# Kernel tuning notes

Hardware: AMD Instinct MI355X
Metric: run time of the kernel (lower is better)

## Reference

```python
import jax, jax.numpy as jnp
import numpy as np

BETA = 0.95
THR = 1.0
SLOPE = 25.0


@jax.custom_vjp
def spike(x):
    # Heaviside spike with fast-sigmoid surrogate gradient (snntorch fast_sigmoid, slope=25)
    return (x > 0).astype(x.dtype)

def _spike_fwd(x):
    return spike(x), x

def _spike_bwd(x, g):
    sg = 1.0 / (SLOPE * jnp.abs(x) + 1.0) ** 2
    return (g * sg,)

spike.defvjp(_spike_fwd, _spike_bwd)


def setup_inputs() -> dict:
    key = jax.random.key(0)
    k_x, k_w1, k_b1, k_w2, k_b2 = jax.random.split(key, 5)
    T, B, D_IN, H, OUT = 30, 4096, 784, 128, 10
    x = jax.random.uniform(k_x, (T, B, D_IN), dtype=jnp.float32)
    # PyTorch nn.Linear default init: U(-1/sqrt(fan_in), 1/sqrt(fan_in))
    lim1 = 1.0 / np.sqrt(D_IN)
    lim2 = 1.0 / np.sqrt(H)
    W1 = jax.random.uniform(k_w1, (H, D_IN), jnp.float32, -lim1, lim1)
    b1 = jax.random.uniform(k_b1, (H,), jnp.float32, -lim1, lim1)
    W2 = jax.random.uniform(k_w2, (OUT, H), jnp.float32, -lim2, lim2)
    b2 = jax.random.uniform(k_b2, (OUT,), jnp.float32, -lim2, lim2)
    return {"x": x, "W1": W1, "b1": b1, "W2": W2, "b2": b2}


def reference(x, W1, b1, W2, b2):
    T, B, _ = x.shape
    H, OUT = W1.shape[0], W2.shape[0]

    def step(carry, xt):
        mem1, mem2 = carry
        # layer 1: linear + leaky integrate-and-fire (reset by subtraction)
        cur1 = xt @ W1.T + b1  # [B, H]
        reset1 = jax.lax.stop_gradient((mem1 - THR > 0).astype(xt.dtype))
        mem1 = BETA * mem1 + cur1 - reset1 * THR
        spk1 = spike(mem1 - THR)
        # layer 2
        cur2 = spk1 @ W2.T + b2  # [B, OUT]
        reset2 = jax.lax.stop_gradient((mem2 - THR > 0).astype(xt.dtype))
        mem2 = BETA * mem2 + cur2 - reset2 * THR
        spk2 = spike(mem2 - THR)
        return (mem1, mem2), (spk2, mem2)

    init = (jnp.zeros((B, H), x.dtype), jnp.zeros((B, OUT), x.dtype))
    _, (spk2_rec, mem2_rec) = jax.lax.scan(step, init, x)
    return spk2_rec, mem2_rec  # each [T, B, OUT]
```

## Files before the change

kernel.cpp:

```cpp
#include <hip/hip_runtime.h>
#include <stdint.h>

#define THR  1.0f
#define BETA 0.95f
#define SX   4096.0f
#define SW   512.0f
#define SINV (1.0f / (4096.0f * 512.0f))
#define W1N  (128 * 784)

typedef __attribute__((ext_vector_type(8)))  _Float16 f16x8;
typedef __attribute__((ext_vector_type(16))) float    f32x16;
typedef __attribute__((ext_vector_type(4)))  float    fvec4;

__device__ __forceinline__ void gll16(const float* g, float* l){
  __builtin_amdgcn_global_load_lds((const __attribute__((address_space(1))) void*)g,
                                   (__attribute__((address_space(3))) void*)l, 16, 0, 0);
}

__global__ void split_w1(const float* __restrict__ W1, _Float16* __restrict__ wB){
  int i = blockIdx.x * 256 + threadIdx.x;
  if (i < W1N) {
    int h = i / 784, k = i % 784;
    float v = W1[i] * SW;
    _Float16 hi = (_Float16)v;
    _Float16 lo = (_Float16)(v - (float)hi);
    int ks = k >> 4, kg = (k >> 3) & 1, j = k & 7, nf = h >> 5, r = h & 31;
    int base = ((ks * 4 + nf) * 2) * 512 + (kg * 32 + r) * 8 + j;
    wB[base]       = hi;
    wB[base + 512] = lo;
  }
}

__launch_bounds__(256, 2)
__global__ void gemm1(const float* __restrict__ x,
                      const float* __restrict__ wBf,
                      const float* __restrict__ b1,
                      float* __restrict__ cur1,
                      long row0){
  __shared__ float lds[20480];
  const int lane = threadIdx.x & 63;
  const int w    = threadIdx.x >> 6;
  const long blk_row0 = row0 + (long)blockIdx.x * 128;
  const int r  = lane & 31;
  const int kg = lane >> 5;
  const int row_a = w * 32 + r;
  const int xr  = (row_a & 7) << 4;
  const int xr3 = (row_a & 3) << 4;

  #define STAGE_A(bb, s) {                                                   \
    _Pragma("unroll") for (int i = 0; i < 4; ++i) {                          \
      int j = w * 4 + i;                                                     \
      int jj = j * 64 + lane;                                   \
      int rw = jj >> 3, q = (jj & 7) << 4;                                   \
      int kb = q ^ ((rw & 7) << 4);                                          \
      gll16(x + (blk_row0 + rw) * 784 + (s) * 32 + (kb >> 2),                \
            &lds[(bb) * 4096 + j * 256]); } }

  #define STAGE_B(bb, p) {                                                   \
    _Pragma("unroll") for (int i = 0; i < 4; ++i) {                          \
      int j = w * 4 + i;                                                     \
      gll16(wBf + (p) * 4096 + j * 256 + lane * 4,                           \
            &lds[8192 + (bb) * 4096 + j * 256]); } }

  #define COMPUTE(bb) {                                                      \
    _Pragma("unroll") for (int ksl = 0; ksl < 2; ++ksl) {                    \
      f16x8 b[8];                                                            \
      _Pragma("unroll") for (int f = 0; f < 8; ++f)                          \
        b[f] = *(const f16x8*)&lds[8192 + (bb) * 4096 + (ksl * 8 + f) * 256 + lane * 4]; \
      int kb0 = ksl * 64 + kg * 32;                                          \
      fvec4 a0 = *(const fvec4*)&lds[(bb) * 4096 + row_a * 32 + (((kb0)      ^ xr) >> 2)]; \
      fvec4 a1 = *(const fvec4*)&lds[(bb) * 4096 + row_a * 32 + (((kb0 + 16) ^ xr) >> 2)]; \
      f16x8 ah, al;                                                          \
      _Pragma("unroll") for (int j = 0; j < 8; ++j) {                        \
        float v = ((j < 4) ? a0[j] : a1[j - 4]) * SX;                        \
        _Float16 hh = (_Float16)v;                                           \
        ah[j] = hh; al[j] = (_Float16)(v - (float)hh);                       \
      }                                                                      \
      _Pragma("unroll") for (int nf = 0; nf < 4; ++nf) {                     \
        acc[nf] = __builtin_amdgcn_mfma_f32_32x32x16_f16(ah, b[nf * 2],     acc[nf], 0, 0, 0); \
        acc[nf] = __builtin_amdgcn_mfma_f32_32x32x16_f16(ah, b[nf * 2 + 1], acc[nf], 0, 0, 0); \
        acc[nf] = __builtin_amdgcn_mfma_f32_32x32x16_f16(al, b[nf * 2],     acc[nf], 0, 0, 0); \
      } } }

  #define FENCE_A() { __builtin_amdgcn_sched_barrier(0);                     \
    asm volatile("s_waitcnt lgkmcnt(0)" ::: "memory");                       \
    __builtin_amdgcn_s_barrier();                                            \
    asm volatile("" ::: "memory"); }
  #define FENCE_B(vm) {                                                      \
    asm volatile("s_waitcnt vmcnt(" #vm ")" ::: "memory");                   \
    __builtin_amdgcn_s_barrier();                                            \
    asm volatile("" ::: "memory");                                           \
    __builtin_amdgcn_sched_barrier(0); }

  f32x16 acc[4] = {};

  #pragma unroll
  for (int i = 0; i < 2; ++i) {
    int j = w * 2 + i;
    int jj = j * 64 + lane;
    int rw = jj >> 2, q = (jj & 3) << 4;
    int kb = q ^ ((rw & 3) << 4);
    gll16(x + (blk_row0 + rw) * 784 + 768 + (kb >> 2), &lds[16384 + j * 256]);
    gll16(wBf + 98304 + j * 256 + lane * 4,            &lds[18432 + j * 256]);
  }
  STAGE_A(0, 0); STAGE_B(0, 0);
  STAGE_A(1, 1); STAGE_B(1, 1);
  FENCE_B(8);
  COMPUTE(0);

  for (int q = 0; q < 11; ++q) {
    const int p1 = 2 * q + 1;
    FENCE_A();
    STAGE_A(0, p1 + 1); STAGE_B(0, p1 + 1);
    FENCE_B(8);
    COMPUTE(1);
    const int p2 = 2 * q + 2;
    FENCE_A();
    STAGE_A(1, p2 + 1); STAGE_B(1, p2 + 1);
    FENCE_B(8);
    COMPUTE(0);
  }

  FENCE_A();
  FENCE_B(0);
  COMPUTE(1);

  {
    f16x8 b[8];
    #pragma unroll
    for (int f = 0; f < 8; ++f)
      b[f] = *(const f16x8*)&lds[18432 + f * 256 + lane * 4];
    int kb0 = kg * 32;
    fvec4 a0 = *(const fvec4*)&lds[16384 + row_a * 16 + (((kb0)      ^ xr3) >> 2)];
    fvec4 a1 = *(const fvec4*)&lds[16384 + row_a * 16 + (((kb0 + 16) ^ xr3) >> 2)];
    f16x8 ah, al;
    #pragma unroll
    for (int j = 0; j < 8; ++j) {
      float v = ((j < 4) ? a0[j] : a1[j - 4]) * SX;
      _Float16 hh = (_Float16)v;
      ah[j] = hh; al[j] = (_Float16)(v - (float)hh);
    }
    #pragma unroll
    for (int nf = 0; nf < 4; ++nf) {
      acc[nf] = __builtin_amdgcn_mfma_f32_32x32x16_f16(ah, b[nf * 2],     acc[nf], 0, 0, 0);
      acc[nf] = __builtin_amdgcn_mfma_f32_32x32x16_f16(ah, b[nf * 2 + 1], acc[nf], 0, 0, 0);
      acc[nf] = __builtin_amdgcn_mfma_f32_32x32x16_f16(al, b[nf * 2],     acc[nf], 0, 0, 0);
    }
  }

  float b1v[4];
  #pragma unroll
  for (int nf = 0; nf < 4; ++nf) b1v[nf] = b1[nf * 32 + r];
  long m0 = (long)blockIdx.x * 128 + w * 32;
  #pragma unroll
  for (int nf = 0; nf < 4; ++nf)
    #pragma unroll
    for (int reg = 0; reg < 16; ++reg) {
      int rr = (reg & 3) + 8 * (reg >> 2) + 4 * kg;
      cur1[(m0 + rr) * 128 + nf * 32 + r] = acc[nf][reg] * SINV + b1v[nf];
    }
  #undef STAGE_A
  #undef STAGE_B
  #undef COMPUTE
  #undef FENCE_A
  #undef FENCE_B
}

__launch_bounds__(256)
__global__ void lif(const float* __restrict__ cur1,
                    const float* __restrict__ W2,
                    const float* __restrict__ b2,
                    float* __restrict__ out,
                    float* __restrict__ state1,
                    float* __restrict__ state2,
                    int t0, int tn){
  const int lane = threadIdx.x & 63;
  const int b = blockIdx.x * 4 + (threadIdx.x >> 6);
  const int o = lane & 15;
  const int c = lane >> 4;

  float wv[32];
  #pragma unroll
  for (int j = 0; j < 32; ++j) wv[j] = 0.f;
  if (o < 10) {
    #pragma unroll
    for (int j = 0; j < 32; ++j) wv[j] = W2[o * 128 + c * 32 + j];
  }
  float b2v = (lane < 10) ? b2[lane] : 0.f;

  float mem1a, mem1b, mem2;
  if (t0 == 0) { mem1a = 0.f; mem1b = 0.f; mem2 = 0.f; }
  else {
    mem1a = state1[b * 128 + lane];
    mem1b = state1[b * 128 + 64 + lane];
    mem2  = (lane < 10) ? state2[b * 10 + lane] : 0.f;
  }

  for (int t = t0; t < tn; ++t) {
    long base = ((long)(t - t0) * 4096 + b) * 128;
    float c1a = cur1[base + lane];
    float c1b = cur1[base + 64 + lane];
    float r1a = (mem1a > THR) ? THR : 0.f;
    float r1b = (mem1b > THR) ? THR : 0.f;
    mem1a = BETA * mem1a + c1a - r1a;
    mem1b = BETA * mem1b + c1b - r1b;

    uint64_t mA = __ballot(mem1a > THR);
    uint64_t mB = __ballot(mem1b > THR);
    uint64_t m64 = (c & 2) ? mB : mA;
    uint32_t bits = (uint32_t)(m64 >> ((c & 1) << 5));

    float s = 0.f;
    #pragma unroll
    for (int j = 0; j < 32; ++j)
      s = fmaf((float)((bits >> j) & 1u), wv[j], s);
    s += __shfl_xor(s, 16);
    s += __shfl_xor(s, 32);

    if (lane < 10) {
      float cur2 = s + b2v;
      float r2 = (mem2 > THR) ? THR : 0.f;
      mem2 = BETA * mem2 + cur2 - r2;
      float s2 = (mem2 > THR) ? 1.f : 0.f;
      long ob = (long)t * 40960 + (long)b * 10 + lane;
      out[ob] = s2;
      out[1228800 + ob] = mem2;
    }
  }

  if (tn < 30) {
    state1[b * 128 + lane] = mem1a;
    state1[b * 128 + 64 + lane] = mem1b;
    if (lane < 10) state2[b * 10 + lane] = mem2;
  }
}

extern "C" void kernel_launch(void* const* d_in, const int* in_sizes, int n_in,
                              void* d_out, int out_size, void* d_ws, size_t ws_size,
                              hipStream_t stream) {
  const float* x  = (const float*)d_in[0];
  const float* W1 = (const float*)d_in[1];
  const float* b1 = (const float*)d_in[2];
  const float* W2 = (const float*)d_in[3];
  const float* b2 = (const float*)d_in[4];
  float* out = (float*)d_out;

  const int T = 30, B = 4096;

  char* ws = (char*)d_ws;
  _Float16* wB = (_Float16*)ws;
  size_t off = (size_t)49 * 8 * 512 * sizeof(_Float16);
  off = (off + 255) & ~(size_t)255;
  float* state1 = (float*)(ws + off); off += (size_t)B * 128 * 4;
  float* state2 = (float*)(ws + off); off += (size_t)B * 10 * 4;
  off = (off + 255) & ~(size_t)255;
  float* cur1 = (float*)(ws + off);

  size_t per_t = (size_t)B * 128 * 4;
  size_t avail = (ws_size > off) ? (ws_size - off) : 0;
  int CH = (int)(avail / per_t);
  if (CH > T) CH = T;
  if (CH < 1) CH = 1;

  split_w1<<<(W1N + 255) / 256, 256, 0, stream>>>(W1, wB);

  for (int t0 = 0; t0 < T; t0 += CH) {
    int tn = (t0 + CH < T) ? (t0 + CH) : T;
    int mrows = (tn - t0) * B;
    gemm1<<<mrows / 128, 256, 0, stream>>>(x, (const float*)wB, b1, cur1, (long)t0 * B);
    lif<<<B / 4, 256, 0, stream>>>(cur1, W2, b2, out, state1, state2, t0, tn);
  }
}
```

Measured before the change: 144.7 us.

## Use four-stage K16 pipeline with direct per-lane A loads in gemm1

Replaces the double-buffered K=32 staging (swizzled A tiles plus a separate tail chunk) with a 4-deep ring of K=16 stages, where each lane loads its own A row fragment straight into LDS in MFMA-ready order. This removes the XOR-swizzle address math and the special K-tail path, and keeps more loads in flight to hide global latency. In exchange there are twice as many barrier rounds per K, smaller 16-byte strided row loads from x, and a lower LDS footprint.

```diff
diff --git a/kernel.cpp b/kernel.cpp
--- a/kernel.cpp
+++ b/kernel.cpp
@@ -37,50 +37,39 @@
                       const float* __restrict__ b1,
                       float* __restrict__ cur1,
                       long row0){
-  __shared__ float lds[20480];
+  __shared__ float lds[16384];
   const int lane = threadIdx.x & 63;
   const int w    = threadIdx.x >> 6;
   const long blk_row0 = row0 + (long)blockIdx.x * 128;
   const int r  = lane & 31;
   const int kg = lane >> 5;
-  const int row_a = w * 32 + r;
-  const int xr  = (row_a & 7) << 4;
-  const int xr3 = (row_a & 3) << 4;
-
-  #define STAGE_A(bb, s) {                                                   \
-    _Pragma("unroll") for (int i = 0; i < 4; ++i) {                          \
-      int j = w * 4 + i;                                                     \
-      int jj = j * 64 + lane;                                   \
-      int rw = jj >> 3, q = (jj & 7) << 4;                                   \
-      int kb = q ^ ((rw & 7) << 4);                                          \
-      gll16(x + (blk_row0 + rw) * 784 + (s) * 32 + (kb >> 2),                \
-            &lds[(bb) * 4096 + j * 256]); } }
-
-  #define STAGE_B(bb, p) {                                                   \
-    _Pragma("unroll") for (int i = 0; i < 4; ++i) {                          \
-      int j = w * 4 + i;                                                     \
-      gll16(wBf + (p) * 4096 + j * 256 + lane * 4,                           \
-            &lds[8192 + (bb) * 4096 + j * 256]); } }
+
+  const float* xA  = x + (blk_row0 + w * 32 + r) * 784 + kg * 8;
+  const float* wBs = wBf + w * 512 + lane * 4;
+
+  #define STAGE(bb, s) {                                                     \
+    gll16(xA  + (s) * 16,       &lds[(bb) * 4096 + (w * 2 + 0) * 256]);      \
+    gll16(xA  + (s) * 16 + 4,   &lds[(bb) * 4096 + (w * 2 + 1) * 256]);      \
+    gll16(wBs + (s) * 2048,     &lds[(bb) * 4096 + 2048 + (w * 2 + 0) * 256]); \
+    gll16(wBs + (s) * 2048 + 256, &lds[(bb) * 4096 + 2048 + (w * 2 + 1) * 256]); }
 
   #define COMPUTE(bb) {                                                      \
-    _Pragma("unroll") for (int ksl = 0; ksl < 2; ++ksl) {                    \
-      f16x8 b[8];                                                            \
-      _Pragma("unroll") for (int f = 0; f < 8; ++f)                          \
-        b[f] = *(const f16x8*)&lds[8192 + (bb) * 4096 + (ksl * 8 + f) * 256 + lane * 4]; \
-      int kb0 = ksl * 64 + kg * 32;                                          \
-      fvec4 a0 = *(const fvec4*)&lds[(bb) * 4096 + row_a * 32 + (((kb0)      ^ xr) >> 2)]; \
-      fvec4 a1 = *(const fvec4*)&lds[(bb) * 4096 + row_a * 32 + (((kb0 + 16) ^ xr) >> 2)]; \
-      f16x8 ah, al;                                                          \
-      _Pragma("unroll") for (int j = 0; j < 8; ++j) {                        \
-        float v = ((j < 4) ? a0[j] : a1[j - 4]) * SX;                        \
-        _Float16 hh = (_Float16)v;                                           \
-        ah[j] = hh; al[j] = (_Float16)(v - (float)hh);                       \
-      }                                                                      \
-      _Pragma("unroll") for (int nf = 0; nf < 4; ++nf) {                     \
-        acc[nf] = __builtin_amdgcn_mfma_f32_32x32x16_f16(ah, b[nf * 2],     acc[nf], 0, 0, 0); \
-        acc[nf] = __builtin_amdgcn_mfma_f32_32x32x16_f16(ah, b[nf * 2 + 1], acc[nf], 0, 0, 0); \
-        acc[nf] = __builtin_amdgcn_mfma_f32_32x32x16_f16(al, b[nf * 2],     acc[nf], 0, 0, 0); \
-      } } }
+    f16x8 b[8];                                                              \
+    _Pragma("unroll") for (int f = 0; f < 8; ++f)                            \
+      b[f] = *(const f16x8*)&lds[(bb) * 4096 + 2048 + f * 256 + lane * 4];   \
+    fvec4 a0 = *(const fvec4*)&lds[(bb) * 4096 + (w * 2 + 0) * 256 + lane * 4]; \
+    fvec4 a1 = *(const fvec4*)&lds[(bb) * 4096 + (w * 2 + 1) * 256 + lane * 4]; \
+    f16x8 ah, al;                                                            \
+    _Pragma("unroll") for (int j = 0; j < 8; ++j) {                          \
+      float v = ((j < 4) ? a0[j] : a1[j - 4]) * SX;                          \
+      _Float16 hh = (_Float16)v;                                             \
+      ah[j] = hh; al[j] = (_Float16)(v - (float)hh);                         \
+    }                                                                        \
+    _Pragma("unroll") for (int nf = 0; nf < 4; ++nf) {                       \
+      acc[nf] = __builtin_amdgcn_mfma_f32_32x32x16_f16(ah, b[nf * 2],     acc[nf], 0, 0, 0); \
+      acc[nf] = __builtin_amdgcn_mfma_f32_32x32x16_f16(ah, b[nf * 2 + 1], acc[nf], 0, 0, 0); \
+      acc[nf] = __builtin_amdgcn_mfma_f32_32x32x16_f16(al, b[nf * 2],     acc[nf], 0, 0, 0); \
+    } }
 
   #define FENCE_A() { __builtin_amdgcn_sched_barrier(0);                     \
     asm volatile("s_waitcnt lgkmcnt(0)" ::: "memory");                       \
@@ -94,59 +83,22 @@
 
   f32x16 acc[4] = {};
 
-  #pragma unroll
-  for (int i = 0; i < 2; ++i) {
-    int j = w * 2 + i;
-    int jj = j * 64 + lane;
-    int rw = jj >> 2, q = (jj & 3) << 4;
-    int kb = q ^ ((rw & 3) << 4);
-    gll16(x + (blk_row0 + rw) * 784 + 768 + (kb >> 2), &lds[16384 + j * 256]);
-    gll16(wBf + 98304 + j * 256 + lane * 4,            &lds[18432 + j * 256]);
-  }
-  STAGE_A(0, 0); STAGE_B(0, 0);
-  STAGE_A(1, 1); STAGE_B(1, 1);
-  FENCE_B(8);
+  STAGE(0, 0); STAGE(1, 1); STAGE(2, 2); STAGE(3, 3);
+  FENCE_B(12);
   COMPUTE(0);
 
   for (int q = 0; q < 11; ++q) {
-    const int p1 = 2 * q + 1;
-    FENCE_A();
-    STAGE_A(0, p1 + 1); STAGE_B(0, p1 + 1);
-    FENCE_B(8);
-    COMPUTE(1);
-    const int p2 = 2 * q + 2;
-    FENCE_A();
-    STAGE_A(1, p2 + 1); STAGE_B(1, p2 + 1);
-    FENCE_B(8);
-    COMPUTE(0);
-  }
-
-  FENCE_A();
-  FENCE_B(0);
-  COMPUTE(1);
-
-  {
-    f16x8 b[8];
-    #pragma unroll
-    for (int f = 0; f < 8; ++f)
-      b[f] = *(const f16x8*)&lds[18432 + f * 256 + lane * 4];
-    int kb0 = kg * 32;
-    fvec4 a0 = *(const fvec4*)&lds[16384 + row_a * 16 + (((kb0)      ^ xr3) >> 2)];
-    fvec4 a1 = *(const fvec4*)&lds[16384 + row_a * 16 + (((kb0 + 16) ^ xr3) >> 2)];
-    f16x8 ah, al;
-    #pragma unroll
-    for (int j = 0; j < 8; ++j) {
-      float v = ((j < 4) ? a0[j] : a1[j - 4]) * SX;
-      _Float16 hh = (_Float16)v;
-      ah[j] = hh; al[j] = (_Float16)(v - (float)hh);
-    }
-    #pragma unroll
-    for (int nf = 0; nf < 4; ++nf) {
-      acc[nf] = __builtin_amdgcn_mfma_f32_32x32x16_f16(ah, b[nf * 2],     acc[nf], 0, 0, 0);
-      acc[nf] = __builtin_amdgcn_mfma_f32_32x32x16_f16(ah, b[nf * 2 + 1], acc[nf], 0, 0, 0);
-      acc[nf] = __builtin_amdgcn_mfma_f32_32x32x16_f16(al, b[nf * 2],     acc[nf], 0, 0, 0);
-    }
-  }
+    const int s = 4 * q + 1;
+    FENCE_A(); STAGE(0, s + 3); FENCE_B(12); COMPUTE(1);
+    FENCE_A(); STAGE(1, s + 4); FENCE_B(12); COMPUTE(2);
+    FENCE_A(); STAGE(2, s + 5); FENCE_B(12); COMPUTE(3);
+    FENCE_A(); STAGE(3, s + 6); FENCE_B(12); COMPUTE(0);
+  }
+
+  FENCE_A(); STAGE(0, 48); FENCE_B(12); COMPUTE(1);
+  FENCE_A();               FENCE_B(8);  COMPUTE(2);
+  FENCE_A();               FENCE_B(4);  COMPUTE(3);
+  FENCE_A();               FENCE_B(0);  COMPUTE(0);
 
   float b1v[4];
   #pragma unroll
@@ -159,8 +111,7 @@
       int rr = (reg & 3) + 8 * (reg >> 2) + 4 * kg;
       cur1[(m0 + rr) * 128 + nf * 32 + r] = acc[nf][reg] * SINV + b1v[nf];
     }
-  #undef STAGE_A
-  #undef STAGE_B
+  #undef STAGE
   #undef COMPUTE
   #undef FENCE_A
   #undef FENCE_B
```

Measured after the change: 172.4 us. 1.19x slower.

## Enlarge gemm1 tile to 256 rows with 8 waves in a 4x2 warp grid

Applied to the files above, without the earlier changes.

The layer-1 GEMM block grows from 128 to 256 rows and from 4 to 8 waves. The waves form a 4x2 grid where each wave computes a 64x64 sub-tile, so every staged W1 tile in LDS is shared by twice as many rows of x. This cuts W1 staging traffic and LDS B-fragment reads per output. In exchange it uses more LDS per block, halves the number of blocks, and changes per-wave register pressure, which may reduce occupancy or latency hiding.

```diff
diff --git a/kernel.cpp b/kernel.cpp
--- a/kernel.cpp
+++ b/kernel.cpp
@@ -31,56 +31,62 @@
   }
 }
 
-__launch_bounds__(256, 2)
+__launch_bounds__(512, 2)
 __global__ void gemm1(const float* __restrict__ x,
                       const float* __restrict__ wBf,
                       const float* __restrict__ b1,
                       float* __restrict__ cur1,
                       long row0){
-  __shared__ float lds[20480];
+  __shared__ float lds[30720];
   const int lane = threadIdx.x & 63;
   const int w    = threadIdx.x >> 6;
-  const long blk_row0 = row0 + (long)blockIdx.x * 128;
+  const int wm   = w >> 1;
+  const int wn   = w & 1;
+  const long blk_row0 = row0 + (long)blockIdx.x * 256;
   const int r  = lane & 31;
   const int kg = lane >> 5;
-  const int row_a = w * 32 + r;
-  const int xr  = (row_a & 7) << 4;
-  const int xr3 = (row_a & 3) << 4;
-
-  #define STAGE_A(bb, s) {                                                   \
-    _Pragma("unroll") for (int i = 0; i < 4; ++i) {                          \
-      int j = w * 4 + i;                                                     \
+  const int row_a = wm * 64;
+
+  #define STAGE_A(p, s) { _Pragma("unroll") for (int i = 0; i < 4; ++i) {    \
+      int j = w * 4 + i;                                          \
       int jj = j * 64 + lane;                                   \
       int rw = jj >> 3, q = (jj & 7) << 4;                                   \
       int kb = q ^ ((rw & 7) << 4);                                          \
       gll16(x + (blk_row0 + rw) * 784 + (s) * 32 + (kb >> 2),                \
-            &lds[(bb) * 4096 + j * 256]); } }
-
-  #define STAGE_B(bb, p) {                                                   \
-    _Pragma("unroll") for (int i = 0; i < 4; ++i) {                          \
-      int j = w * 4 + i;                                                     \
-      gll16(wBf + (p) * 4096 + j * 256 + lane * 4,                           \
-            &lds[8192 + (bb) * 4096 + j * 256]); } }
-
-  #define COMPUTE(bb) {                                                      \
-    _Pragma("unroll") for (int ksl = 0; ksl < 2; ++ksl) {                    \
-      f16x8 b[8];                                                            \
-      _Pragma("unroll") for (int f = 0; f < 8; ++f)                          \
-        b[f] = *(const f16x8*)&lds[8192 + (bb) * 4096 + (ksl * 8 + f) * 256 + lane * 4]; \
-      int kb0 = ksl * 64 + kg * 32;                                          \
-      fvec4 a0 = *(const fvec4*)&lds[(bb) * 4096 + row_a * 32 + (((kb0)      ^ xr) >> 2)]; \
-      fvec4 a1 = *(const fvec4*)&lds[(bb) * 4096 + row_a * 32 + (((kb0 + 16) ^ xr) >> 2)]; \
+            &lds[(p) * 8192 + j * 256]); } }
+
+  #define STAGE_B(p, s) { _Pragma("unroll") for (int i = 0; i < 2; ++i) {    \
+      int j = w * 2 + i;                                          \
+      gll16(wBf + (s) * 4096 + j * 256 + lane * 4,                           \
+            &lds[16384 + (p) * 4096 + j * 256]); } }
+
+  #define STAGE(p, s) { STAGE_A(p, s); STAGE_B(p, s); }
+
+  #define KSTEP(p, ksl) {                                                    \
+    f16x8 b[4];                                                              \
+    _Pragma("unroll") for (int nfl = 0; nfl < 2; ++nfl)                      \
+      _Pragma("unroll") for (int t = 0; t < 2; ++t)                          \
+        b[nfl * 2 + t] = *(const f16x8*)&lds[16384 + (p) * 4096 +            \
+            ((ksl) * 8 + (wn * 2 + nfl) * 2 + t) * 256 + lane * 4];          \
+    _Pragma("unroll") for (int mf = 0; mf < 2; ++mf) {                       \
+      int ra = row_a + mf * 32 + r;                                          \
+      int xr = (ra & 7) << 4;                                                \
+      int kb0 = (ksl) * 64 + kg * 32;                                        \
+      fvec4 a0 = *(const fvec4*)&lds[(p) * 8192 + ra * 32 + (((kb0)      ^ xr) >> 2)]; \
+      fvec4 a1 = *(const fvec4*)&lds[(p) * 8192 + ra * 32 + (((kb0 + 16) ^ xr) >> 2)]; \
       f16x8 ah, al;                                                          \
       _Pragma("unroll") for (int j = 0; j < 8; ++j) {                        \
         float v = ((j < 4) ? a0[j] : a1[j - 4]) * SX;                        \
         _Float16 hh = (_Float16)v;                                           \
         ah[j] = hh; al[j] = (_Float16)(v - (float)hh);                       \
       }                                                                      \
-      _Pragma("unroll") for (int nf = 0; nf < 4; ++nf) {                     \
-        acc[nf] = __builtin_amdgcn_mfma_f32_32x32x16_f16(ah, b[nf * 2],     acc[nf], 0, 0, 0); \
-        acc[nf] = __builtin_amdgcn_mfma_f32_32x32x16_f16(ah, b[nf * 2 + 1], acc[nf], 0, 0, 0); \
-        acc[nf] = __builtin_amdgcn_mfma_f32_32x32x16_f16(al, b[nf * 2],     acc[nf], 0, 0, 0); \
+      _Pragma("unroll") for (int nfl = 0; nfl < 2; ++nfl) {                  \
+        acc[mf * 2 + nfl] = __builtin_amdgcn_mfma_f32_32x32x16_f16(ah, b[nfl * 2],     acc[mf * 2 + nfl], 0, 0, 0); \
+        acc[mf * 2 + nfl] = __builtin_amdgcn_mfma_f32_32x32x16_f16(ah, b[nfl * 2 + 1], acc[mf * 2 + nfl], 0, 0, 0); \
+        acc[mf * 2 + nfl] = __builtin_amdgcn_mfma_f32_32x32x16_f16(al, b[nfl * 2],     acc[mf * 2 + nfl], 0, 0, 0); \
       } } }
+
+  #define CPH(p) { KSTEP(p, 0); KSTEP(p, 1); }
 
   #define FENCE_A() { __builtin_amdgcn_sched_barrier(0);                     \
     asm volatile("s_waitcnt lgkmcnt(0)" ::: "memory");                       \
@@ -100,68 +106,71 @@
     int jj = j * 64 + lane;
     int rw = jj >> 2, q = (jj & 3) << 4;
     int kb = q ^ ((rw & 3) << 4);
-    gll16(x + (blk_row0 + rw) * 784 + 768 + (kb >> 2), &lds[16384 + j * 256]);
-    gll16(wBf + 98304 + j * 256 + lane * 4,            &lds[18432 + j * 256]);
-  }
-  STAGE_A(0, 0); STAGE_B(0, 0);
-  STAGE_A(1, 1); STAGE_B(1, 1);
-  FENCE_B(8);
-  COMPUTE(0);
+    gll16(x + (blk_row0 + rw) * 784 + 768 + (kb >> 2), &lds[24576 + j * 256]);
+  }
+  gll16(wBf + 24 * 4096 + w * 256 + lane * 4, &lds[28672 + w * 256]);
+  STAGE(0, 0);
+  STAGE(1, 1);
+  FENCE_B(6);
+  CPH(0);
 
   for (int q = 0; q < 11; ++q) {
-    const int p1 = 2 * q + 1;
-    FENCE_A();
-    STAGE_A(0, p1 + 1); STAGE_B(0, p1 + 1);
-    FENCE_B(8);
-    COMPUTE(1);
-    const int p2 = 2 * q + 2;
-    FENCE_A();
-    STAGE_A(1, p2 + 1); STAGE_B(1, p2 + 1);
-    FENCE_B(8);
-    COMPUTE(0);
-  }
-
+    const int s = 2 * q + 1;
+    FENCE_A(); STAGE(0, s + 1); FENCE_B(6); CPH(1);
+    FENCE_A(); STAGE(1, s + 2); FENCE_B(6); CPH(0);
+  }
   FENCE_A();
   FENCE_B(0);
-  COMPUTE(1);
-
+  CPH(1);
   {
-    f16x8 b[8];
-    #pragma unroll
-    for (int f = 0; f < 8; ++f)
-      b[f] = *(const f16x8*)&lds[18432 + f * 256 + lane * 4];
-    int kb0 = kg * 32;
-    fvec4 a0 = *(const fvec4*)&lds[16384 + row_a * 16 + (((kb0)      ^ xr3) >> 2)];
-    fvec4 a1 = *(const fvec4*)&lds[16384 + row_a * 16 + (((kb0 + 16) ^ xr3) >> 2)];
-    f16x8 ah, al;
-    #pragma unroll
-    for (int j = 0; j < 8; ++j) {
-      float v = ((j < 4) ? a0[j] : a1[j - 4]) * SX;
-      _Float16 hh = (_Float16)v;
-      ah[j] = hh; al[j] = (_Float16)(v - (float)hh);
+    f16x8 b[4];
+    #pragma unroll
+    for (int nfl = 0; nfl < 2; ++nfl)
+      #pragma unroll
+      for (int t = 0; t < 2; ++t)
+        b[nfl * 2 + t] = *(const f16x8*)&lds[28672 + ((wn * 2 + nfl) * 2 + t) * 256 + lane * 4];
+    #pragma unroll
+    for (int mf = 0; mf < 2; ++mf) {
+      int ra = row_a + mf * 32 + r;
+      int xr3 = (ra & 3) << 4;
+      int kb0 = kg * 32;
+      fvec4 a0 = *(const fvec4*)&lds[24576 + ra * 16 + (((kb0)      ^ xr3) >> 2)];
+      fvec4 a1 = *(const fvec4*)&lds[24576 + ra * 16 + (((kb0 + 16) ^ xr3) >> 2)];
+      f16x8 ah, al;
+      #pragma unroll
+      for (int j = 0; j < 8; ++j) {
+        float v = ((j < 4) ? a0[j] : a1[j - 4]) * SX;
+        _Float16 hh = (_Float16)v;
+        ah[j] = hh; al[j] = (_Float16)(v - (float)hh);
+      }
+      #pragma unroll
+      for (int nfl = 0; nfl < 2; ++nfl) {
+        acc[mf * 2 + nfl] = __builtin_amdgcn_mfma_f32_32x32x16_f16(ah, b[nfl * 2],     acc[mf * 2 + nfl], 0, 0, 0);
+        acc[mf * 2 + nfl] = __builtin_amdgcn_mfma_f32_32x32x16_f16(ah, b[nfl * 2 + 1], acc[mf * 2 + nfl], 0, 0, 0);
+        acc[mf * 2 + nfl] = __builtin_amdgcn_mfma_f32_32x32x16_f16(al, b[nfl * 2],     acc[mf * 2 + nfl], 0, 0, 0);
+      }
     }
-    #pragma unroll
-    for (int nf = 0; nf < 4; ++nf) {
-      acc[nf] = __builtin_amdgcn_mfma_f32_32x32x16_f16(ah, b[nf * 2],     acc[nf], 0, 0, 0);
-      acc[nf] = __builtin_amdgcn_mfma_f32_32x32x16_f16(ah, b[nf * 2 + 1], acc[nf], 0, 0, 0);
-      acc[nf] = __builtin_amdgcn_mfma_f32_32x32x16_f16(al, b[nf * 2],     acc[nf], 0, 0, 0);
-    }
-  }
-
-  float b1v[4];
-  #pragma unroll
-  for (int nf = 0; nf < 4; ++nf) b1v[nf] = b1[nf * 32 + r];
-  long m0 = (long)blockIdx.x * 128 + w * 32;
-  #pragma unroll
-  for (int nf = 0; nf < 4; ++nf)
-    #pragma unroll
-    for (int reg = 0; reg < 16; ++reg) {
-      int rr = (reg & 3) + 8 * (reg >> 2) + 4 * kg;
-      cur1[(m0 + rr) * 128 + nf * 32 + r] = acc[nf][reg] * SINV + b1v[nf];
-    }
+  }
+
+  float b1v[2];
+  #pragma unroll
+  for (int nfl = 0; nfl < 2; ++nfl) b1v[nfl] = b1[wn * 64 + nfl * 32 + r];
+  long m0 = (long)blockIdx.x * 256 + wm * 64;
+  #pragma unroll
+  for (int mf = 0; mf < 2; ++mf)
+    #pragma unroll
+    for (int nfl = 0; nfl < 2; ++nfl)
+      #pragma unroll
+      for (int reg = 0; reg < 16; ++reg) {
+        int rr = (reg & 3) + 8 * (reg >> 2) + 4 * kg;
+        cur1[(m0 + mf * 32 + rr) * 128 + wn * 64 + nfl * 32 + r] =
+            acc[mf * 2 + nfl][reg] * SINV + b1v[nfl];
+      }
   #undef STAGE_A
   #undef STAGE_B
-  #undef COMPUTE
+  #undef STAGE
+  #undef KSTEP
+  #undef CPH
   #undef FENCE_A
   #undef FENCE_B
 }
@@ -267,7 +276,7 @@
   for (int t0 = 0; t0 < T; t0 += CH) {
     int tn = (t0 + CH < T) ? (t0 + CH) : T;
     int mrows = (tn - t0) * B;
-    gemm1<<<mrows / 128, 256, 0, stream>>>(x, (const float*)wB, b1, cur1, (long)t0 * B);
+    gemm1<<<mrows / 256, 512, 0, stream>>>(x, (const float*)wB, b1, cur1, (long)t0 * B);
     lif<<<B / 4, 256, 0, stream>>>(cur1, W2, b2, out, state1, state2, t0, tn);
   }
 }
```

Result: slower. 154.0 us (+6.4%).
